# Kernel tuning notes

Hardware: AMD Instinct MI355X
Metric: run time of the kernel (lower is better)

Reference implementation:

```python
import jax, jax.numpy as jnp
import numpy as np

N_NODES = 20000
N_EDGES = 320000
DIM = 256
OUT_DIM = 256
N_LAYERS = 2
AVG_LOG = float(np.log(17.0))  # PNA avg_deg['log'] from deg histogram (all degree 16)
STD_EPS = 1e-5
N_AGG = 5
N_SCALER = 3


def _pna_conv(x, edge_index, Wpre, bpre, Wpost, bpost, Wlin, blin):
    """PyG PNAConv (towers=1, pre_layers=1, post_layers=1, divide_input=False)."""
    N = x.shape[0]
    src, dst = edge_index[0], edge_index[1]  # messages flow src -> dst
    # pre_nn on concat([x_i, x_j]) per edge: [E, 2F] -> [E, F]
    m = jnp.concatenate([x[dst], x[src]], axis=-1) @ Wpre.T + bpre
    deg = jax.ops.segment_sum(jnp.ones((src.shape[0],), x.dtype), dst, num_segments=N)
    degc = jnp.maximum(deg, 1.0)[:, None]
    s = jax.ops.segment_sum(m, dst, num_segments=N)
    mean = s / degc
    mean2 = jax.ops.segment_sum(m * m, dst, num_segments=N) / degc
    std = jnp.sqrt(jax.nn.relu(mean2 - mean * mean) + STD_EPS)
    has = (deg > 0)[:, None]
    mn = jnp.where(has, jax.ops.segment_min(m, dst, num_segments=N), 0.0)
    mx = jnp.where(has, jax.ops.segment_max(m, dst, num_segments=N), 0.0)
    agg = jnp.concatenate([mean, s, std, mn, mx], axis=-1)  # [N, 5F]
    logd = jnp.log(degc + 1.0)
    scaled = jnp.concatenate(
        [agg, agg * (logd / AVG_LOG), agg * (AVG_LOG / logd)], axis=-1)  # [N, 15F]
    h = jnp.concatenate([x, scaled], axis=-1) @ Wpost.T + bpost  # [N, F_out]
    return h @ Wlin.T + blin


def setup_inputs() -> dict:
    key = jax.random.key(0)
    ks = jax.random.split(key, 20)
    F = DIM
    L = N_LAYERS
    post_in = (N_AGG * N_SCALER + 1) * F  # 16F = 4096
    sc = 0.05
    inp = {
        "x": jax.random.normal(ks[0], (N_NODES, F), jnp.float32),
        "edge_index_in": jax.random.randint(ks[1], (2, N_EDGES), 0, N_NODES),
        "edge_index_out": jax.random.randint(ks[2], (2, N_EDGES), 0, N_NODES),
    }
    def p(k, shape):
        return sc * jax.random.normal(k, shape, jnp.float32)
    # stacked per-layer params; supply (_s) and demand (_d) channels
    for tag, base in (("s", 3), ("d", 9)):
        inp[f"Wpre_{tag}"] = p(ks[base + 0], (L, F, 2 * F))
        inp[f"bpre_{tag}"] = p(ks[base + 1], (L, F))
        inp[f"Wpost_{tag}"] = p(ks[base + 2], (L, OUT_DIM, post_in))
        inp[f"bpost_{tag}"] = p(ks[base + 3], (L, OUT_DIM))
        inp[f"Wlin_{tag}"] = p(ks[base + 4], (L, OUT_DIM, OUT_DIM))
        inp[f"blin_{tag}"] = p(ks[base + 5], (L, OUT_DIM))
    inp["Wcomb"] = p(ks[15], (L, OUT_DIM, F + 2 * OUT_DIM))
    inp["bcomb"] = p(ks[16], (L, OUT_DIM))
    inp["Wout"] = p(ks[17], (1, OUT_DIM))
    inp["bout"] = p(ks[18], (1,))
    return inp


def reference(x, edge_index_in, edge_index_out,
              Wpre_s, bpre_s, Wpost_s, bpost_s, Wlin_s, blin_s,
              Wpre_d, bpre_d, Wpost_d, bpost_d, Wlin_d, blin_d,
              Wcomb, bcomb, Wout, bout):
    for l in range(N_LAYERS):
        h_in = jax.nn.relu(_pna_conv(x, edge_index_in,
                                     Wpre_s[l], bpre_s[l], Wpost_s[l], bpost_s[l],
                                     Wlin_s[l], blin_s[l]))
        h_out = jax.nn.relu(_pna_conv(x, edge_index_out,
                                      Wpre_d[l], bpre_d[l], Wpost_d[l], bpost_d[l],
                                      Wlin_d[l], blin_d[l]))
        x = jax.nn.relu(jnp.concatenate([x, h_in, h_out], axis=-1) @ Wcomb[l].T + bcomb[l])
    return jnp.squeeze(x @ Wout.T + bout)  # [N]
```

## Files before the change

### kernel.cpp

```cpp
#include <hip/hip_runtime.h>
#include <math.h>

#define NN 20000
#define NE 320000
#define FD 256
#define AVG_LOG_F 2.83321334f

typedef unsigned short u16;
typedef _Float16 h8_t __attribute__((ext_vector_type(8)));
typedef float f4_t __attribute__((ext_vector_type(4)));

__device__ __forceinline__ u16 f2h(float f) {
  _Float16 h = (_Float16)f;
  return __builtin_bit_cast(u16, h);
}
__device__ __forceinline__ float h2f(u16 u) {
  _Float16 h = __builtin_bit_cast(_Float16, u);
  return (float)h;
}
__device__ __forceinline__ void gld16(const void* g, void* l) {
  __builtin_amdgcn_global_load_lds(
      (const __attribute__((address_space(1))) void*)g,
      (__attribute__((address_space(3))) void*)l, 16, 0, 0);
}

__global__ __launch_bounds__(256) void k_count(const int* __restrict__ dst,
                                               int* __restrict__ deg, int E) {
  int e = blockIdx.x * 256 + threadIdx.x;
  if (e < E) atomicAdd(&deg[dst[e]], 1);
}

__global__ __launch_bounds__(1024) void k_scan(const int* __restrict__ deg,
                                               int* __restrict__ rp, int N) {
  __shared__ int lds[1024];
  int t = threadIdx.x;
  int CH = (N + 1023) >> 10;
  int base = t * CH;
  int s = 0;
  for (int i = 0; i < CH; ++i) { int idx = base + i; if (idx < N) s += deg[idx]; }
  lds[t] = s;
  __syncthreads();
  for (int off = 1; off < 1024; off <<= 1) {
    int v = (t >= off) ? lds[t - off] : 0;
    __syncthreads();
    lds[t] += v;
    __syncthreads();
  }
  int run = (t == 0) ? 0 : lds[t - 1];
  for (int i = 0; i < CH; ++i) {
    int idx = base + i;
    if (idx < N) { rp[idx] = run; run += deg[idx]; }
  }
  if (t == 1023) rp[N] = run;
}

__global__ __launch_bounds__(256) void k_scatter(const int* __restrict__ src,
                                                 const int* __restrict__ dst,
                                                 const int* __restrict__ rp,
                                                 int* __restrict__ cur,
                                                 int* __restrict__ col, int E) {
  int e = blockIdx.x * 256 + threadIdx.x;
  if (e < E) {
    int d = dst[e];
    int p = atomicAdd(&cur[d], 1);
    col[rp[d] + p] = src[e];
  }
}

__global__ __launch_bounds__(256) void k_cvt(const float* __restrict__ in,
                                             u16* __restrict__ out, int n4) {
  int i = blockIdx.x * 256 + threadIdx.x;
  if (i < n4) {
    float4 v = *(const float4*)(in + (size_t)i * 4);
    ushort4 o;
    o.x = f2h(v.x); o.y = f2h(v.y); o.z = f2h(v.z); o.w = f2h(v.w);
    *(ushort4*)(out + (size_t)i * 4) = o;
  }
}

__global__ __launch_bounds__(256) void k_cvtx(const float* __restrict__ x,
                                              u16* __restrict__ xc) {
  int i = blockIdx.x * 256 + threadIdx.x;
  int row = i >> 6, c = (i & 63) * 4;
  float4 v = *(const float4*)(x + (size_t)row * 256 + c);
  ushort4 o;
  o.x = f2h(v.x); o.y = f2h(v.y); o.z = f2h(v.z); o.w = f2h(v.w);
  *(ushort4*)(xc + (size_t)row * 768 + c) = o;
}

__global__ __launch_bounds__(256) void k_tc(const float* __restrict__ in,
                                            u16* __restrict__ out) {
  __shared__ float tile[32][33];
  int bx = blockIdx.x;
  int by = blockIdx.y;
  int r = threadIdx.x >> 5, c = threadIdx.x & 31;
#pragma unroll
  for (int it = 0; it < 4; ++it)
    tile[r + it * 8][c] = in[(size_t)(by * 32 + r + it * 8) * 4096 + bx * 32 + c];
  __syncthreads();
#pragma unroll
  for (int it = 0; it < 4; ++it)
    out[(size_t)(bx * 32 + r + it * 8) * 256 + by * 32 + c] = f2h(tile[c][r + it * 8]);
}

__global__ __launch_bounds__(512) void k_mgemm(
    const u16* __restrict__ A, int lda,
    const u16* __restrict__ B, const u16* __restrict__ B2, int ldb, int nsplit,
    const float* __restrict__ bias, const float* __restrict__ bias2,
    float* __restrict__ oF, int ldoF, int ncutF,
    u16* __restrict__ oH, int ldoH,
    int M, int K, int relu) {
  __shared__ u16 As[64 * 64];
  __shared__ u16 Bs[256 * 64];
  const int t = threadIdx.x;
  const int m0 = blockIdx.y * 64;
  const int n0 = blockIdx.x * 256;
  const int l = t & 63;
  const int w = t >> 6;
  const int wm = w >> 2, wn = w & 3;
  const int lo = l & 15, hi = l >> 4;

  f4_t acc[2][4];
#pragma unroll
  for (int i = 0; i < 2; ++i)
#pragma unroll
    for (int j = 0; j < 4; ++j) acc[i][j] = (f4_t)0.f;

  int ra = t >> 3, pa = t & 7;
  int la = pa ^ (ra & 7);
  int rra = m0 + ra;
  if (rra > M - 1) rra = M - 1;
  const u16* gA = A + (size_t)rra * lda + la * 8;
  u16* lA = &As[t * 8];

  const u16* gB[4];
  u16* lB[4];
#pragma unroll
  for (int i = 0; i < 4; ++i) {
    int q = i * 512 + t;
    int r = q >> 3, p = q & 7;
    int lc = p ^ (r & 7);
    int n = n0 + r;
    const u16* bp = (n < nsplit) ? (B + (size_t)n * ldb)
                                 : (B2 + (size_t)(n - nsplit) * ldb);
    gB[i] = bp + lc * 8;
    lB[i] = &Bs[q * 8];
  }

  for (int k0 = 0; k0 < K; k0 += 64) {
    gld16(gA + k0, lA);
#pragma unroll
    for (int i = 0; i < 4; ++i) gld16(gB[i] + k0, lB[i]);
    __syncthreads();
#pragma unroll
    for (int ks = 0; ks < 2; ++ks) {
      h8_t af[2], bf[4];
#pragma unroll
      for (int mi = 0; mi < 2; ++mi) {
        int row = wm * 32 + mi * 16 + lo;
        int c = (ks * 4 + hi) ^ (row & 7);
        af[mi] = *(const h8_t*)&As[row * 64 + c * 8];
      }
#pragma unroll
      for (int ni = 0; ni < 4; ++ni) {
        int row = wn * 64 + ni * 16 + lo;
        int c = (ks * 4 + hi) ^ (row & 7);
        bf[ni] = *(const h8_t*)&Bs[row * 64 + c * 8];
      }
#pragma unroll
      for (int mi = 0; mi < 2; ++mi)
#pragma unroll
        for (int ni = 0; ni < 4; ++ni)
          acc[mi][ni] = __builtin_amdgcn_mfma_f32_16x16x32_f16(
              af[mi], bf[ni], acc[mi][ni], 0, 0, 0);
    }
    __syncthreads();
  }

  float bv[4];
#pragma unroll
  for (int ni = 0; ni < 4; ++ni) {
    int n = n0 + wn * 64 + ni * 16 + lo;
    bv[ni] = (n < nsplit) ? (bias ? bias[n] : 0.f)
                          : (bias2 ? bias2[n - nsplit] : 0.f);
  }
#pragma unroll
  for (int mi = 0; mi < 2; ++mi) {
#pragma unroll
    for (int r = 0; r < 4; ++r) {
      int m = m0 + wm * 32 + mi * 16 + hi * 4 + r;
      if (m < M) {
#pragma unroll
        for (int ni = 0; ni < 4; ++ni) {
          int n = n0 + wn * 64 + ni * 16 + lo;
          float v = acc[mi][ni][r] + bv[ni];
          if (relu && v < 0.f) v = 0.f;
          if (n < ncutF) {
            oF[(size_t)m * ldoF + n] = v;
          } else {
            oH[(size_t)m * ldoH + (n - ncutF)] = f2h(v);
          }
        }
      }
    }
  }
}

__global__ __launch_bounds__(512) void k_pgemm(
    const u16* __restrict__ xc, const u16* __restrict__ agg5,
    const float* __restrict__ scal3, const u16* __restrict__ Wf,
    const float* __restrict__ bf, u16* __restrict__ oH, int M) {
  __shared__ u16 As[64 * 64];
  __shared__ u16 Bs[256 * 64];
  const int t = threadIdx.x;
  const int m0 = blockIdx.x * 64;
  const int l = t & 63;
  const int w = t >> 6;
  const int wm = w >> 2, wn = w & 3;
  const int lo = l & 15, hi = l >> 4;

  f4_t acc[2][4];
#pragma unroll
  for (int i = 0; i < 2; ++i)
#pragma unroll
    for (int j = 0; j < 4; ++j) acc[i][j] = (f4_t)0.f;

  const int ra = t >> 3, pa = t & 7;
  int m = m0 + ra;
  if (m > M - 1) m = M - 1;
  u16* ldA = &As[ra * 64 + (pa ^ (ra & 7)) * 8];
  const u16* xrow = xc + (size_t)m * 768;
  const u16* arow = agg5 + (size_t)m * 1280;
  const float* srow = scal3 + (size_t)m * 4;

  const u16* gB[4];
  u16* lB[4];
#pragma unroll
  for (int i = 0; i < 4; ++i) {
    int q = i * 512 + t;
    int r = q >> 3, p = q & 7;
    int lc = p ^ (r & 7);
    gB[i] = Wf + (size_t)r * 4096 + lc * 8;
    lB[i] = &Bs[q * 8];
  }

  for (int k0 = 0; k0 < 4096; k0 += 64) {
#pragma unroll
    for (int i = 0; i < 4; ++i) gld16(gB[i] + k0, lB[i]);
    int k = k0 + pa * 8;
    h8_t v;
    if (k < 256) {
      v = *(const h8_t*)(xrow + k);
    } else {
      int q = k - 256;
      int g = q / 1280;
      int r2 = q - g * 1280;
      v = *(const h8_t*)(arow + r2);
      v = v * (_Float16)srow[g];
    }
    *(h8_t*)ldA = v;
    __syncthreads();
#pragma unroll
    for (int ks = 0; ks < 2; ++ks) {
      h8_t af[2], bfr[4];
#pragma unroll
      for (int mi = 0; mi < 2; ++mi) {
        int row = wm * 32 + mi * 16 + lo;
        int c = (ks * 4 + hi) ^ (row & 7);
        af[mi] = *(const h8_t*)&As[row * 64 + c * 8];
      }
#pragma unroll
      for (int ni = 0; ni < 4; ++ni) {
        int row = wn * 64 + ni * 16 + lo;
        int c = (ks * 4 + hi) ^ (row & 7);
        bfr[ni] = *(const h8_t*)&Bs[row * 64 + c * 8];
      }
#pragma unroll
      for (int mi = 0; mi < 2; ++mi)
#pragma unroll
        for (int ni = 0; ni < 4; ++ni)
          acc[mi][ni] = __builtin_amdgcn_mfma_f32_16x16x32_f16(
              af[mi], bfr[ni], acc[mi][ni], 0, 0, 0);
    }
    __syncthreads();
  }

  float bv[4];
#pragma unroll
  for (int ni = 0; ni < 4; ++ni) bv[ni] = bf[wn * 64 + ni * 16 + lo];
#pragma unroll
  for (int mi = 0; mi < 2; ++mi) {
#pragma unroll
    for (int r = 0; r < 4; ++r) {
      int mr = m0 + wm * 32 + mi * 16 + hi * 4 + r;
      if (mr < M) {
#pragma unroll
        for (int ni = 0; ni < 4; ++ni) {
          int n = wn * 64 + ni * 16 + lo;
          float vv = acc[mi][ni][r] + bv[ni];
          if (vv < 0.f) vv = 0.f;
          oH[(size_t)mr * 768 + n] = f2h(vv);
        }
      }
    }
  }
}

__global__ __launch_bounds__(256) void k_aggregate(
    const float* __restrict__ A, const u16* __restrict__ Bh,
    const int* __restrict__ rp, const int* __restrict__ col,
    u16* __restrict__ agg5, float* __restrict__ scal3) {
  int w = threadIdx.x >> 6, l = threadIdx.x & 63;
  int n = blockIdx.x * 4 + w;
  int beg = rp[n], end = rp[n + 1];
  int deg = end - beg;
  float sb[4] = {0.f, 0.f, 0.f, 0.f}, qb[4] = {0.f, 0.f, 0.f, 0.f};
  float mnb[4], mxb[4];
#pragma unroll
  for (int j = 0; j < 4; ++j) { mnb[j] = 3.402823466e38f; mxb[j] = -3.402823466e38f; }
  for (int i = beg; i < end; ++i) {
    int s = col[i];
    ushort4 bv = *(const ushort4*)(Bh + (size_t)s * FD + l * 4);
    float b[4] = {h2f(bv.x), h2f(bv.y), h2f(bv.z), h2f(bv.w)};
#pragma unroll
    for (int j = 0; j < 4; ++j) {
      sb[j] += b[j];
      qb[j] = fmaf(b[j], b[j], qb[j]);
      mnb[j] = fminf(mnb[j], b[j]);
      mxb[j] = fmaxf(mxb[j], b[j]);
    }
  }
  float4 c4 = *(const float4*)(A + (size_t)n * FD + l * 4);
  float cc[4] = {c4.x, c4.y, c4.z, c4.w};
  float degf = (float)deg;
  float degc = degf > 1.f ? degf : 1.f;
  float inv = 1.f / degc;
  float outv[5][4];
#pragma unroll
  for (int j = 0; j < 4; ++j) {
    float c = cc[j];
    float s_m = fmaf(degf, c, sb[j]);
    float mean = s_m * inv;
    float mean2 = fmaf(degf * c, c, fmaf(2.f * c, sb[j], qb[j])) * inv;
    float var = mean2 - mean * mean;
    if (var < 0.f) var = 0.f;
    float sd = sqrtf(var + 1e-5f);
    outv[0][j] = mean;
    outv[1][j] = s_m;
    outv[2][j] = sd;
    outv[3][j] = deg > 0 ? c + mnb[j] : 0.f;
    outv[4][j] = deg > 0 ? c + mxb[j] : 0.f;
  }
  u16* base = agg5 + (size_t)n * 1280 + l * 4;
#pragma unroll
  for (int a = 0; a < 5; ++a) {
    ushort4 o;
    o.x = f2h(outv[a][0]);
    o.y = f2h(outv[a][1]);
    o.z = f2h(outv[a][2]);
    o.w = f2h(outv[a][3]);
    *(ushort4*)(base + a * 256) = o;
  }
  if (l == 0) {
    float logd = logf(degc + 1.f);
    scal3[(size_t)n * 4 + 0] = 1.f;
    scal3[(size_t)n * 4 + 1] = logd / AVG_LOG_F;
    scal3[(size_t)n * 4 + 2] = AVG_LOG_F / logd;
    scal3[(size_t)n * 4 + 3] = 0.f;
  }
}

__global__ __launch_bounds__(256) void k_bfuse(const float* __restrict__ Wlin,
                                               const float* __restrict__ bpost,
                                               const float* __restrict__ blin,
                                               float* __restrict__ bf) {
  __shared__ float bp[256];
  int t = threadIdx.x;
  bp[t] = bpost[t];
  __syncthreads();
  float s = blin[t];
  for (int k = 0; k < 256; ++k) s = fmaf(Wlin[t * 256 + k], bp[k], s);
  bf[t] = s;
}

__global__ __launch_bounds__(256) void k_wout(const u16* __restrict__ x,
                                              const float* __restrict__ w,
                                              const float* __restrict__ b,
                                              float* __restrict__ out, int N) {
  int wid = threadIdx.x >> 6, lane = threadIdx.x & 63;
  int n = blockIdx.x * 4 + wid;
  if (n >= N) return;
  ushort4 xv = *(const ushort4*)(x + (size_t)n * FD + lane * 4);
  const float4 wv = *(const float4*)(w + lane * 4);
  float s = h2f(xv.x) * wv.x + h2f(xv.y) * wv.y + h2f(xv.z) * wv.z + h2f(xv.w) * wv.w;
#pragma unroll
  for (int off = 32; off > 0; off >>= 1) s += __shfl_down(s, off);
  if (lane == 0) out[n] = s + b[0];
}

extern "C" void kernel_launch(void* const* d_in, const int* in_sizes, int n_in,
                              void* d_out, int out_size, void* d_ws, size_t ws_size,
                              hipStream_t stream) {
  const float* x0      = (const float*)d_in[0];
  const int*   ei_in   = (const int*)d_in[1];
  const int*   ei_out  = (const int*)d_in[2];
  const float* Wpre_s  = (const float*)d_in[3];
  const float* bpre_s  = (const float*)d_in[4];
  const float* Wpost_s = (const float*)d_in[5];
  const float* bpost_s = (const float*)d_in[6];
  const float* Wlin_s  = (const float*)d_in[7];
  const float* blin_s  = (const float*)d_in[8];
  const float* Wpre_d  = (const float*)d_in[9];
  const float* bpre_d  = (const float*)d_in[10];
  const float* Wpost_d = (const float*)d_in[11];
  const float* bpost_d = (const float*)d_in[12];
  const float* Wlin_d  = (const float*)d_in[13];
  const float* blin_d  = (const float*)d_in[14];
  const float* Wcomb   = (const float*)d_in[15];
  const float* bcomb   = (const float*)d_in[16];
  const float* Wout    = (const float*)d_in[17];
  const float* bout    = (const float*)d_in[18];
  float* out = (float*)d_out;

  char* p = (char*)d_ws;
  auto alloc = [&](size_t b) {
    char* r = p;
    p += (b + 255) & ~(size_t)255;
    return r;
  };
  int* deg      = (int*)alloc((size_t)NN * 4);
  int* cur      = (int*)alloc((size_t)NN * 4);
  int* rp_in    = (int*)alloc((size_t)(NN + 1) * 4);
  int* col_in   = (int*)alloc((size_t)NE * 4);
  int* rp_out   = (int*)alloc((size_t)(NN + 1) * 4);
  int* col_out  = (int*)alloc((size_t)NE * 4);
  float* Abuf   = (float*)alloc((size_t)NN * FD * 4);
  u16* Bbuf     = (u16*)alloc((size_t)NN * FD * 2);
  u16* agg5     = (u16*)alloc((size_t)NN * 1280 * 2);
  float* scal3  = (float*)alloc((size_t)NN * 4 * 4);
  u16* xcat1    = (u16*)alloc((size_t)NN * 768 * 2);
  u16* xcat2    = (u16*)alloc((size_t)NN * 768 * 2);
  u16* xfin     = (u16*)alloc((size_t)NN * FD * 2);
  u16* Wpre_sb  = (u16*)alloc((size_t)2 * 256 * 512 * 2);
  u16* Wpre_db  = (u16*)alloc((size_t)2 * 256 * 512 * 2);
  u16* Wlin_sb  = (u16*)alloc((size_t)2 * 256 * 256 * 2);
  u16* Wlin_db  = (u16*)alloc((size_t)2 * 256 * 256 * 2);
  u16* Wcomb_b  = (u16*)alloc((size_t)2 * 256 * 768 * 2);
  u16* WpostT   = (u16*)alloc((size_t)4096 * 256 * 2);
  u16* Wf       = (u16*)alloc((size_t)256 * 4096 * 2);
  float* bfv    = (float*)alloc((size_t)256 * 4);

  const int EB = (NE + 255) / 256;
  const int BIG = 1 << 30;

  k_cvt<<<256, 256, 0, stream>>>(Wpre_s, Wpre_sb, 65536);
  k_cvt<<<256, 256, 0, stream>>>(Wpre_d, Wpre_db, 65536);
  k_cvt<<<128, 256, 0, stream>>>(Wlin_s, Wlin_sb, 32768);
  k_cvt<<<128, 256, 0, stream>>>(Wlin_d, Wlin_db, 32768);
  k_cvt<<<384, 256, 0, stream>>>(Wcomb, Wcomb_b, 98304);
  k_cvtx<<<5000, 256, 0, stream>>>(x0, xcat1);

  hipMemsetAsync(deg, 0, (size_t)NN * 4, stream);
  k_count<<<EB, 256, 0, stream>>>(ei_in + NE, deg, NE);
  k_scan<<<1, 1024, 0, stream>>>(deg, rp_in, NN);
  hipMemsetAsync(cur, 0, (size_t)NN * 4, stream);
  k_scatter<<<EB, 256, 0, stream>>>(ei_in, ei_in + NE, rp_in, cur, col_in, NE);
  hipMemsetAsync(deg, 0, (size_t)NN * 4, stream);
  k_count<<<EB, 256, 0, stream>>>(ei_out + NE, deg, NE);
  k_scan<<<1, 1024, 0, stream>>>(deg, rp_out, NN);
  hipMemsetAsync(cur, 0, (size_t)NN * 4, stream);
  k_scatter<<<EB, 256, 0, stream>>>(ei_out, ei_out + NE, rp_out, cur, col_out, NE);

  u16* xcats[2] = {xcat1, xcat2};
  for (int lyr = 0; lyr < 2; ++lyr) {
    u16* xc = xcats[lyr];
    for (int c = 0; c < 2; ++c) {
      const float* bpre  = (c == 0) ? bpre_s : bpre_d;
      const float* Wpost = (c == 0) ? Wpost_s : Wpost_d;
      const float* bpost = (c == 0) ? bpost_s : bpost_d;
      const float* Wlin  = (c == 0) ? Wlin_s : Wlin_d;
      const float* blin  = (c == 0) ? blin_s : blin_d;
      u16* Wpre_b = (c == 0) ? Wpre_sb : Wpre_db;
      u16* Wlin_b = (c == 0) ? Wlin_sb : Wlin_db;
      const int* rp  = (c == 0) ? rp_in : rp_out;
      const int* col = (c == 0) ? col_in : col_out;

      k_mgemm<<<dim3(2, 313), 512, 0, stream>>>(
          xc, 768,
          Wpre_b + (size_t)lyr * 131072, Wpre_b + (size_t)lyr * 131072 + 256, 512, 256,
          bpre + (size_t)lyr * 256, nullptr,
          Abuf, 256, 256,
          Bbuf, 256,
          NN, 256, 0);
      k_aggregate<<<5000, 256, 0, stream>>>(Abuf, Bbuf, rp, col, agg5, scal3);
      k_tc<<<dim3(128, 8), 256, 0, stream>>>(Wpost + (size_t)lyr * 256 * 4096, WpostT);
      k_mgemm<<<dim3(16, 4), 512, 0, stream>>>(
          Wlin_b + (size_t)lyr * 65536, 256,
          WpostT, WpostT, 256, BIG,
          nullptr, nullptr,
          nullptr, 0, 0,
          Wf, 4096,
          256, 256, 0);
      k_bfuse<<<1, 256, 0, stream>>>(Wlin + (size_t)lyr * 65536,
                                     bpost + (size_t)lyr * 256,
                                     blin + (size_t)lyr * 256, bfv);
      k_pgemm<<<dim3(313), 512, 0, stream>>>(
          xc, agg5, scal3, Wf, bfv, xc + 256 + c * 256, NN);
    }
    if (lyr == 0) {
      k_mgemm<<<dim3(1, 313), 512, 0, stream>>>(
          xc, 768,
          Wcomb_b, Wcomb_b, 768, BIG,
          bcomb, nullptr,
          nullptr, 0, 0,
          xcat2, 768,
          NN, 768, 1);
    } else {
      k_mgemm<<<dim3(1, 313), 512, 0, stream>>>(
          xc, 768,
          Wcomb_b + 196608, Wcomb_b + 196608, 768, BIG,
          bcomb + 256, nullptr,
          nullptr, 0, 0,
          xfin, 256,
          NN, 768, 1);
    }
  }
  k_wout<<<5000, 256, 0, stream>>>(xfin, Wout, bout, out, NN);
}
```

Measured before the change: 937.6 us.

## Batch setup kernels, double-buffer GEMMs, fuse channels, fp16 pre-GEMM outputs

Merges the weight conversions, degree counting, CSR scatter, Wpost transposes, weight folding and bias folding into single batched launches covering both channels and both layers. Adds LDS double buffering to the GEMM and post-GEMM kernels so global loads overlap with MFMA work. Runs both channels' post-GEMMs in one launch. The pre-GEMM now writes both halves in fp16, and the aggregation reads 8 halves per lane with two edges in flight per wave. The trade-offs are lower precision in the center term, double the LDS per block (possibly lower occupancy), and buffer aliasing (WpostT4 in agg52, xfin in xcat1) that relies on stream ordering.

After: 852.4 us. 9.1% less time.

```diff
diff --git a/kernel.cpp b/kernel.cpp
--- a/kernel.cpp
+++ b/kernel.cpp
@@ -3,7 +3,6 @@
 
 #define NN 20000
 #define NE 320000
-#define FD 256
 #define AVG_LOG_F 2.83321334f
 
 typedef unsigned short u16;
@@ -13,10 +12,6 @@
 __device__ __forceinline__ u16 f2h(float f) {
   _Float16 h = (_Float16)f;
   return __builtin_bit_cast(u16, h);
-}
-__device__ __forceinline__ float h2f(u16 u) {
-  _Float16 h = __builtin_bit_cast(_Float16, u);
-  return (float)h;
 }
 __device__ __forceinline__ void gld16(const void* g, void* l) {
   __builtin_amdgcn_global_load_lds(
@@ -24,10 +19,13 @@
       (__attribute__((address_space(3))) void*)l, 16, 0, 0);
 }
 
-__global__ __launch_bounds__(256) void k_count(const int* __restrict__ dst,
-                                               int* __restrict__ deg, int E) {
+__global__ __launch_bounds__(256) void k_count2(const int* __restrict__ ein,
+                                                const int* __restrict__ eout,
+                                                int* __restrict__ deg2, int E) {
   int e = blockIdx.x * 256 + threadIdx.x;
-  if (e < E) atomicAdd(&deg[dst[e]], 1);
+  int ch = blockIdx.y;
+  const int* dst = (ch ? eout : ein) + E;
+  if (e < E) atomicAdd(&deg2[ch * NN + dst[e]], 1);
 }
 
 __global__ __launch_bounds__(1024) void k_scan(const int* __restrict__ deg,
@@ -54,28 +52,44 @@
   if (t == 1023) rp[N] = run;
 }
 
-__global__ __launch_bounds__(256) void k_scatter(const int* __restrict__ src,
-                                                 const int* __restrict__ dst,
-                                                 const int* __restrict__ rp,
-                                                 int* __restrict__ cur,
-                                                 int* __restrict__ col, int E) {
+__global__ __launch_bounds__(256) void k_scatter2(const int* __restrict__ ein,
+                                                  const int* __restrict__ eout,
+                                                  const int* __restrict__ rp2,
+                                                  int* __restrict__ cur2,
+                                                  int* __restrict__ col2, int E) {
   int e = blockIdx.x * 256 + threadIdx.x;
+  int ch = blockIdx.y;
+  const int* src = (ch ? eout : ein);
+  const int* dst = src + E;
   if (e < E) {
     int d = dst[e];
-    int p = atomicAdd(&cur[d], 1);
-    col[rp[d] + p] = src[e];
-  }
-}
-
-__global__ __launch_bounds__(256) void k_cvt(const float* __restrict__ in,
-                                             u16* __restrict__ out, int n4) {
+    int p = atomicAdd(&cur2[ch * NN + d], 1);
+    col2[rp2[ch * NN + d] + p] = src[e];
+  }
+}
+
+__global__ __launch_bounds__(256) void k_cvtw(
+    const float* __restrict__ Wpre_s, const float* __restrict__ Wpre_d,
+    const float* __restrict__ Wlin_s, const float* __restrict__ Wlin_d,
+    const float* __restrict__ Wcomb,
+    u16* __restrict__ preS, u16* __restrict__ preD,
+    u16* __restrict__ lincat, u16* __restrict__ combB) {
   int i = blockIdx.x * 256 + threadIdx.x;
-  if (i < n4) {
-    float4 v = *(const float4*)(in + (size_t)i * 4);
-    ushort4 o;
-    o.x = f2h(v.x); o.y = f2h(v.y); o.z = f2h(v.z); o.w = f2h(v.w);
-    *(ushort4*)(out + (size_t)i * 4) = o;
-  }
+  const float* src;
+  u16* dst;
+  int so, dofs;
+  if (i < 65536)       { src = Wpre_s; dst = preS;  so = i;          dofs = so; }
+  else if (i < 131072) { src = Wpre_d; dst = preD;  so = i - 65536;  dofs = so; }
+  else if (i < 163840) { int j = i - 131072; int lyr = j >> 14;
+                         src = Wlin_s; dst = lincat; so = j; dofs = j + lyr * 16384; }
+  else if (i < 196608) { int j = i - 163840; int lyr = j >> 14;
+                         src = Wlin_d; dst = lincat; so = j; dofs = j + (lyr + 1) * 16384; }
+  else if (i < 294912) { src = Wcomb; dst = combB; so = i - 196608; dofs = so; }
+  else return;
+  float4 v = *(const float4*)(src + (size_t)so * 4);
+  ushort4 o;
+  o.x = f2h(v.x); o.y = f2h(v.y); o.z = f2h(v.z); o.w = f2h(v.w);
+  *(ushort4*)(dst + (size_t)dofs * 4) = o;
 }
 
 __global__ __launch_bounds__(256) void k_cvtx(const float* __restrict__ x,
@@ -88,11 +102,14 @@
   *(ushort4*)(xc + (size_t)row * 768 + c) = o;
 }
 
-__global__ __launch_bounds__(256) void k_tc(const float* __restrict__ in,
-                                            u16* __restrict__ out) {
+__global__ __launch_bounds__(256) void k_tc4(const float* __restrict__ Ws,
+                                             const float* __restrict__ Wd,
+                                             u16* __restrict__ outT) {
   __shared__ float tile[32][33];
-  int bx = blockIdx.x;
-  int by = blockIdx.y;
+  int z = blockIdx.z;
+  const float* in = ((z & 1) ? Wd : Ws) + (size_t)(z >> 1) * 256 * 4096;
+  u16* out = outT + (size_t)z * (4096 * 256);
+  int bx = blockIdx.x, by = blockIdx.y;
   int r = threadIdx.x >> 5, c = threadIdx.x & 31;
 #pragma unroll
   for (int it = 0; it < 4; ++it)
@@ -106,17 +123,20 @@
 __global__ __launch_bounds__(512) void k_mgemm(
     const u16* __restrict__ A, int lda,
     const u16* __restrict__ B, const u16* __restrict__ B2, int ldb, int nsplit,
-    const float* __restrict__ bias, const float* __restrict__ bias2,
-    float* __restrict__ oF, int ldoF, int ncutF,
+    const float* __restrict__ bias,
     u16* __restrict__ oH, int ldoH,
-    int M, int K, int relu) {
-  __shared__ u16 As[64 * 64];
-  __shared__ u16 Bs[256 * 64];
+    int M, int K, int relu, int zA, int zB, int zO) {
+  __shared__ u16 As[2][64 * 64];
+  __shared__ u16 Bs[2][256 * 64];
   const int t = threadIdx.x;
+  const int z = blockIdx.z;
+  A += (size_t)z * zA;
+  B += (size_t)z * zB;
+  B2 += (size_t)z * zB;
+  oH += (size_t)z * zO;
   const int m0 = blockIdx.y * 64;
   const int n0 = blockIdx.x * 256;
-  const int l = t & 63;
-  const int w = t >> 6;
+  const int l = t & 63, w = t >> 6;
   const int wm = w >> 2, wn = w & 3;
   const int lo = l & 15, hi = l >> 4;
 
@@ -126,53 +146,60 @@
 #pragma unroll
     for (int j = 0; j < 4; ++j) acc[i][j] = (f4_t)0.f;
 
-  int ra = t >> 3, pa = t & 7;
-  int la = pa ^ (ra & 7);
+  const int ra = t >> 3, pa = t & 7;
+  const int la = pa ^ (ra & 7);
   int rra = m0 + ra;
   if (rra > M - 1) rra = M - 1;
   const u16* gA = A + (size_t)rra * lda + la * 8;
-  u16* lA = &As[t * 8];
 
   const u16* gB[4];
-  u16* lB[4];
+  int lBo[4];
 #pragma unroll
   for (int i = 0; i < 4; ++i) {
     int q = i * 512 + t;
-    int r = q >> 3, p = q & 7;
-    int lc = p ^ (r & 7);
+    int r = q >> 3, p2 = q & 7;
+    int lc = p2 ^ (r & 7);
     int n = n0 + r;
-    const u16* bp = (n < nsplit) ? (B + (size_t)n * ldb)
-                                 : (B2 + (size_t)(n - nsplit) * ldb);
+    const u16* bp = (n < nsplit) ? (B + (size_t)n * ldb) : (B2 + (size_t)(n - nsplit) * ldb);
     gB[i] = bp + lc * 8;
-    lB[i] = &Bs[q * 8];
-  }
-
-  for (int k0 = 0; k0 < K; k0 += 64) {
-    gld16(gA + k0, lA);
-#pragma unroll
-    for (int i = 0; i < 4; ++i) gld16(gB[i] + k0, lB[i]);
-    __syncthreads();
+    lBo[i] = q * 8;
+  }
+
+  gld16(gA, &As[0][t * 8]);
+#pragma unroll
+  for (int i = 0; i < 4; ++i) gld16(gB[i], &Bs[0][lBo[i]]);
+  __syncthreads();
+
+  const int nt = K >> 6;
+  for (int tt = 0; tt < nt; ++tt) {
+    const int cur = tt & 1;
+    if (tt + 1 < nt) {
+      const int ko = (tt + 1) << 6;
+      gld16(gA + ko, &As[cur ^ 1][t * 8]);
+#pragma unroll
+      for (int i = 0; i < 4; ++i) gld16(gB[i] + ko, &Bs[cur ^ 1][lBo[i]]);
+    }
 #pragma unroll
     for (int ks = 0; ks < 2; ++ks) {
-      h8_t af[2], bf[4];
+      h8_t af[2], bfr[4];
 #pragma unroll
       for (int mi = 0; mi < 2; ++mi) {
         int row = wm * 32 + mi * 16 + lo;
         int c = (ks * 4 + hi) ^ (row & 7);
-        af[mi] = *(const h8_t*)&As[row * 64 + c * 8];
+        af[mi] = *(const h8_t*)&As[cur][row * 64 + c * 8];
       }
 #pragma unroll
       for (int ni = 0; ni < 4; ++ni) {
         int row = wn * 64 + ni * 16 + lo;
         int c = (ks * 4 + hi) ^ (row & 7);
-        bf[ni] = *(const h8_t*)&Bs[row * 64 + c * 8];
+        bfr[ni] = *(const h8_t*)&Bs[cur][row * 64 + c * 8];
       }
 #pragma unroll
       for (int mi = 0; mi < 2; ++mi)
 #pragma unroll
         for (int ni = 0; ni < 4; ++ni)
           acc[mi][ni] = __builtin_amdgcn_mfma_f32_16x16x32_f16(
-              af[mi], bf[ni], acc[mi][ni], 0, 0, 0);
+              af[mi], bfr[ni], acc[mi][ni], 0, 0, 0);
     }
     __syncthreads();
   }
@@ -181,8 +208,7 @@
 #pragma unroll
   for (int ni = 0; ni < 4; ++ni) {
     int n = n0 + wn * 64 + ni * 16 + lo;
-    bv[ni] = (n < nsplit) ? (bias ? bias[n] : 0.f)
-                          : (bias2 ? bias2[n - nsplit] : 0.f);
+    bv[ni] = (n < nsplit) ? (bias ? bias[n] : 0.f) : 0.f;
   }
 #pragma unroll
   for (int mi = 0; mi < 2; ++mi) {
@@ -195,11 +221,7 @@
           int n = n0 + wn * 64 + ni * 16 + lo;
           float v = acc[mi][ni][r] + bv[ni];
           if (relu && v < 0.f) v = 0.f;
-          if (n < ncutF) {
-            oF[(size_t)m * ldoF + n] = v;
-          } else {
-            oH[(size_t)m * ldoH + (n - ncutF)] = f2h(v);
-          }
+          oH[(size_t)m * ldoH + n] = f2h(v);
         }
       }
     }
@@ -207,15 +229,20 @@
 }
 
 __global__ __launch_bounds__(512) void k_pgemm(
-    const u16* __restrict__ xc, const u16* __restrict__ agg5,
-    const float* __restrict__ scal3, const u16* __restrict__ Wf,
-    const float* __restrict__ bf, u16* __restrict__ oH, int M) {
-  __shared__ u16 As[64 * 64];
-  __shared__ u16 Bs[256 * 64];
+    const u16* __restrict__ xc, const u16* __restrict__ agg5c,
+    const float* __restrict__ scal3c, const u16* __restrict__ Wfl,
+    const float* __restrict__ bfl, u16* __restrict__ oHb, int M) {
+  __shared__ u16 As[2][64 * 64];
+  __shared__ u16 Bs[2][256 * 64];
   const int t = threadIdx.x;
+  const int ch = blockIdx.y;
+  const u16* agg5 = agg5c + (size_t)ch * NN * 1280;
+  const float* scal3 = scal3c + (size_t)ch * NN * 4;
+  const u16* Wf = Wfl + (size_t)ch * (256 * 4096);
+  const float* bf = bfl + ch * 256;
+  u16* oH = oHb + 256 + ch * 256;
   const int m0 = blockIdx.x * 64;
-  const int l = t & 63;
-  const int w = t >> 6;
+  const int l = t & 63, w = t >> 6;
   const int wm = w >> 2, wn = w & 3;
   const int lo = l & 15, hi = l >> 4;
 
@@ -228,38 +255,50 @@
   const int ra = t >> 3, pa = t & 7;
   int m = m0 + ra;
   if (m > M - 1) m = M - 1;
-  u16* ldA = &As[ra * 64 + (pa ^ (ra & 7)) * 8];
   const u16* xrow = xc + (size_t)m * 768;
   const u16* arow = agg5 + (size_t)m * 1280;
-  const float* srow = scal3 + (size_t)m * 4;
+  const float s1 = scal3[(size_t)m * 4 + 1];
+  const float s2 = scal3[(size_t)m * 4 + 2];
+  const int aslot = ra * 64 + (pa ^ (ra & 7)) * 8;
 
   const u16* gB[4];
-  u16* lB[4];
+  int lBo[4];
 #pragma unroll
   for (int i = 0; i < 4; ++i) {
     int q = i * 512 + t;
-    int r = q >> 3, p = q & 7;
-    int lc = p ^ (r & 7);
+    int r = q >> 3, p2 = q & 7;
+    int lc = p2 ^ (r & 7);
     gB[i] = Wf + (size_t)r * 4096 + lc * 8;
-    lB[i] = &Bs[q * 8];
-  }
-
-  for (int k0 = 0; k0 < 4096; k0 += 64) {
-#pragma unroll
-    for (int i = 0; i < 4; ++i) gld16(gB[i] + k0, lB[i]);
-    int k = k0 + pa * 8;
-    h8_t v;
-    if (k < 256) {
-      v = *(const h8_t*)(xrow + k);
-    } else {
-      int q = k - 256;
-      int g = q / 1280;
-      int r2 = q - g * 1280;
-      v = *(const h8_t*)(arow + r2);
-      v = v * (_Float16)srow[g];
-    }
-    *(h8_t*)ldA = v;
-    __syncthreads();
+    lBo[i] = q * 8;
+  }
+
+  {
+    h8_t va = *(const h8_t*)(xrow + pa * 8);
+#pragma unroll
+    for (int i = 0; i < 4; ++i) gld16(gB[i], &Bs[0][lBo[i]]);
+    *(h8_t*)&As[0][aslot] = va;
+  }
+  __syncthreads();
+
+  for (int tt = 0; tt < 64; ++tt) {
+    const int cur = tt & 1;
+    h8_t va2 = (h8_t)(_Float16)0.f;
+    float fac = 1.f;
+    if (tt < 63) {
+      int k = ((tt + 1) << 6) + pa * 8;
+      const u16* ap;
+      if (k < 256) {
+        ap = xrow + k;
+      } else {
+        int q = k - 256;
+        int r2 = q < 1280 ? q : (q < 2560 ? q - 1280 : q - 2560);
+        fac = q < 1280 ? 1.f : (q < 2560 ? s1 : s2);
+        ap = arow + r2;
+      }
+      va2 = *(const h8_t*)ap;
+#pragma unroll
+      for (int i = 0; i < 4; ++i) gld16(gB[i] + ((tt + 1) << 6), &Bs[cur ^ 1][lBo[i]]);
+    }
 #pragma unroll
     for (int ks = 0; ks < 2; ++ks) {
       h8_t af[2], bfr[4];
@@ -267,13 +306,13 @@
       for (int mi = 0; mi < 2; ++mi) {
         int row = wm * 32 + mi * 16 + lo;
         int c = (ks * 4 + hi) ^ (row & 7);
-        af[mi] = *(const h8_t*)&As[row * 64 + c * 8];
+        af[mi] = *(const h8_t*)&As[cur][row * 64 + c * 8];
       }
 #pragma unroll
       for (int ni = 0; ni < 4; ++ni) {
         int row = wn * 64 + ni * 16 + lo;
         int c = (ks * 4 + hi) ^ (row & 7);
-        bfr[ni] = *(const h8_t*)&Bs[row * 64 + c * 8];
+        bfr[ni] = *(const h8_t*)&Bs[cur][row * 64 + c * 8];
       }
 #pragma unroll
       for (int mi = 0; mi < 2; ++mi)
@@ -282,6 +321,7 @@
           acc[mi][ni] = __builtin_amdgcn_mfma_f32_16x16x32_f16(
               af[mi], bfr[ni], acc[mi][ni], 0, 0, 0);
     }
+    if (tt < 63) *(h8_t*)&As[cur ^ 1][aslot] = va2 * (_Float16)fac;
     __syncthreads();
   }
 
@@ -307,80 +347,92 @@
 }
 
 __global__ __launch_bounds__(256) void k_aggregate(
-    const float* __restrict__ A, const u16* __restrict__ Bh,
-    const int* __restrict__ rp, const int* __restrict__ col,
-    u16* __restrict__ agg5, float* __restrict__ scal3) {
+    const u16* __restrict__ AB, const int* __restrict__ rp,
+    const int* __restrict__ col, u16* __restrict__ agg5,
+    float* __restrict__ scal3) {
   int w = threadIdx.x >> 6, l = threadIdx.x & 63;
   int n = blockIdx.x * 4 + w;
   int beg = rp[n], end = rp[n + 1];
   int deg = end - beg;
-  float sb[4] = {0.f, 0.f, 0.f, 0.f}, qb[4] = {0.f, 0.f, 0.f, 0.f};
-  float mnb[4], mxb[4];
-#pragma unroll
-  for (int j = 0; j < 4; ++j) { mnb[j] = 3.402823466e38f; mxb[j] = -3.402823466e38f; }
-  for (int i = beg; i < end; ++i) {
+  int half = l >> 5, lf = l & 31;
+  float sb[8], qb[8], mnb[8], mxb[8];
+#pragma unroll
+  for (int j = 0; j < 8; ++j) {
+    sb[j] = 0.f; qb[j] = 0.f;
+    mnb[j] = 3.402823466e38f; mxb[j] = -3.402823466e38f;
+  }
+  for (int i = beg + half; i < end; i += 2) {
     int s = col[i];
-    ushort4 bv = *(const ushort4*)(Bh + (size_t)s * FD + l * 4);
-    float b[4] = {h2f(bv.x), h2f(bv.y), h2f(bv.z), h2f(bv.w)};
-#pragma unroll
-    for (int j = 0; j < 4; ++j) {
-      sb[j] += b[j];
-      qb[j] = fmaf(b[j], b[j], qb[j]);
-      mnb[j] = fminf(mnb[j], b[j]);
-      mxb[j] = fmaxf(mxb[j], b[j]);
-    }
-  }
-  float4 c4 = *(const float4*)(A + (size_t)n * FD + l * 4);
-  float cc[4] = {c4.x, c4.y, c4.z, c4.w};
+    h8_t bv = *(const h8_t*)(AB + (size_t)s * 512 + 256 + lf * 8);
+#pragma unroll
+    for (int j = 0; j < 8; ++j) {
+      float b = (float)bv[j];
+      sb[j] += b;
+      qb[j] = fmaf(b, b, qb[j]);
+      mnb[j] = fminf(mnb[j], b);
+      mxb[j] = fmaxf(mxb[j], b);
+    }
+  }
+#pragma unroll
+  for (int j = 0; j < 8; ++j) {
+    sb[j] += __shfl_xor(sb[j], 32, 64);
+    qb[j] += __shfl_xor(qb[j], 32, 64);
+    mnb[j] = fminf(mnb[j], __shfl_xor(mnb[j], 32, 64));
+    mxb[j] = fmaxf(mxb[j], __shfl_xor(mxb[j], 32, 64));
+  }
+  h8_t cv = *(const h8_t*)(AB + (size_t)n * 512 + lf * 8);
   float degf = (float)deg;
   float degc = degf > 1.f ? degf : 1.f;
   float inv = 1.f / degc;
-  float outv[5][4];
-#pragma unroll
-  for (int j = 0; j < 4; ++j) {
-    float c = cc[j];
+  float ov[5][8];
+#pragma unroll
+  for (int j = 0; j < 8; ++j) {
+    float c = (float)cv[j];
     float s_m = fmaf(degf, c, sb[j]);
     float mean = s_m * inv;
     float mean2 = fmaf(degf * c, c, fmaf(2.f * c, sb[j], qb[j])) * inv;
     float var = mean2 - mean * mean;
     if (var < 0.f) var = 0.f;
     float sd = sqrtf(var + 1e-5f);
-    outv[0][j] = mean;
-    outv[1][j] = s_m;
-    outv[2][j] = sd;
-    outv[3][j] = deg > 0 ? c + mnb[j] : 0.f;
-    outv[4][j] = deg > 0 ? c + mxb[j] : 0.f;
-  }
-  u16* base = agg5 + (size_t)n * 1280 + l * 4;
-#pragma unroll
-  for (int a = 0; a < 5; ++a) {
-    ushort4 o;
-    o.x = f2h(outv[a][0]);
-    o.y = f2h(outv[a][1]);
-    o.z = f2h(outv[a][2]);
-    o.w = f2h(outv[a][3]);
-    *(ushort4*)(base + a * 256) = o;
-  }
-  if (l == 0) {
-    float logd = logf(degc + 1.f);
-    scal3[(size_t)n * 4 + 0] = 1.f;
-    scal3[(size_t)n * 4 + 1] = logd / AVG_LOG_F;
-    scal3[(size_t)n * 4 + 2] = AVG_LOG_F / logd;
-    scal3[(size_t)n * 4 + 3] = 0.f;
-  }
-}
-
-__global__ __launch_bounds__(256) void k_bfuse(const float* __restrict__ Wlin,
-                                               const float* __restrict__ bpost,
-                                               const float* __restrict__ blin,
-                                               float* __restrict__ bf) {
+    ov[0][j] = mean;
+    ov[1][j] = s_m;
+    ov[2][j] = sd;
+    ov[3][j] = deg > 0 ? c + mnb[j] : 0.f;
+    ov[4][j] = deg > 0 ? c + mxb[j] : 0.f;
+  }
+  if (half == 0) {
+    u16* base = agg5 + (size_t)n * 1280 + lf * 8;
+#pragma unroll
+    for (int a = 0; a < 5; ++a) {
+      h8_t o;
+#pragma unroll
+      for (int j = 0; j < 8; ++j) o[j] = (_Float16)ov[a][j];
+      *(h8_t*)(base + a * 256) = o;
+    }
+    if (lf == 0) {
+      float logd = logf(degc + 1.f);
+      float4 sc = make_float4(1.f, logd / AVG_LOG_F, AVG_LOG_F / logd, 0.f);
+      *(float4*)(scal3 + (size_t)n * 4) = sc;
+    }
+  }
+}
+
+__global__ __launch_bounds__(256) void k_bfuse4(
+    const float* __restrict__ Wlin_s, const float* __restrict__ Wlin_d,
+    const float* __restrict__ bpost_s, const float* __restrict__ bpost_d,
+    const float* __restrict__ blin_s, const float* __restrict__ blin_d,
+    float* __restrict__ bfv4) {
   __shared__ float bp[256];
+  int z = blockIdx.x, lyr = z >> 1, ch = z & 1;
+  const float* Wlin = (ch ? Wlin_d : Wlin_s) + (size_t)lyr * 65536;
+  const float* bpost = (ch ? bpost_d : bpost_s) + lyr * 256;
+  const float* blin = (ch ? blin_d : blin_s) + lyr * 256;
   int t = threadIdx.x;
   bp[t] = bpost[t];
   __syncthreads();
   float s = blin[t];
   for (int k = 0; k < 256; ++k) s = fmaf(Wlin[t * 256 + k], bp[k], s);
-  bf[t] = s;
+  bfv4[z * 256 + t] = s;
 }
 
 __global__ __launch_bounds__(256) void k_wout(const u16* __restrict__ x,
@@ -390,9 +442,12 @@
   int wid = threadIdx.x >> 6, lane = threadIdx.x & 63;
   int n = blockIdx.x * 4 + wid;
   if (n >= N) return;
-  ushort4 xv = *(const ushort4*)(x + (size_t)n * FD + lane * 4);
+  ushort4 xv = *(const ushort4*)(x + (size_t)n * 256 + lane * 4);
   const float4 wv = *(const float4*)(w + lane * 4);
-  float s = h2f(xv.x) * wv.x + h2f(xv.y) * wv.y + h2f(xv.z) * wv.z + h2f(xv.w) * wv.w;
+  float s = (float)__builtin_bit_cast(_Float16, xv.x) * wv.x +
+            (float)__builtin_bit_cast(_Float16, xv.y) * wv.y +
+            (float)__builtin_bit_cast(_Float16, xv.z) * wv.z +
+            (float)__builtin_bit_cast(_Float16, xv.w) * wv.w;
 #pragma unroll
   for (int off = 32; off > 0; off >>= 1) s += __shfl_down(s, off);
   if (lane == 0) out[n] = s + b[0];
@@ -428,101 +483,63 @@
     p += (b + 255) & ~(size_t)255;
     return r;
   };
-  int* deg      = (int*)alloc((size_t)NN * 4);
-  int* cur      = (int*)alloc((size_t)NN * 4);
-  int* rp_in    = (int*)alloc((size_t)(NN + 1) * 4);
-  int* col_in   = (int*)alloc((size_t)NE * 4);
-  int* rp_out   = (int*)alloc((size_t)(NN + 1) * 4);
-  int* col_out  = (int*)alloc((size_t)NE * 4);
-  float* Abuf   = (float*)alloc((size_t)NN * FD * 4);
-  u16* Bbuf     = (u16*)alloc((size_t)NN * FD * 2);
-  u16* agg5     = (u16*)alloc((size_t)NN * 1280 * 2);
-  float* scal3  = (float*)alloc((size_t)NN * 4 * 4);
+  int* deg2     = (int*)alloc((size_t)2 * NN * 4);
+  int* cur2     = (int*)alloc((size_t)2 * NN * 4);
+  int* rp2      = (int*)alloc((size_t)(2 * NN + 1) * 4);
+  int* col2     = (int*)alloc((size_t)2 * NE * 4);
+  u16* AB       = (u16*)alloc((size_t)NN * 512 * 2);
+  u16* agg52    = (u16*)alloc((size_t)2 * NN * 1280 * 2);
+  float* scal32 = (float*)alloc((size_t)2 * NN * 4 * 4);
   u16* xcat1    = (u16*)alloc((size_t)NN * 768 * 2);
   u16* xcat2    = (u16*)alloc((size_t)NN * 768 * 2);
-  u16* xfin     = (u16*)alloc((size_t)NN * FD * 2);
-  u16* Wpre_sb  = (u16*)alloc((size_t)2 * 256 * 512 * 2);
-  u16* Wpre_db  = (u16*)alloc((size_t)2 * 256 * 512 * 2);
-  u16* Wlin_sb  = (u16*)alloc((size_t)2 * 256 * 256 * 2);
-  u16* Wlin_db  = (u16*)alloc((size_t)2 * 256 * 256 * 2);
-  u16* Wcomb_b  = (u16*)alloc((size_t)2 * 256 * 768 * 2);
-  u16* WpostT   = (u16*)alloc((size_t)4096 * 256 * 2);
-  u16* Wf       = (u16*)alloc((size_t)256 * 4096 * 2);
-  float* bfv    = (float*)alloc((size_t)256 * 4);
-
-  const int EB = (NE + 255) / 256;
+  u16* preS     = (u16*)alloc((size_t)2 * 256 * 512 * 2);
+  u16* preD     = (u16*)alloc((size_t)2 * 256 * 512 * 2);
+  u16* lincat   = (u16*)alloc((size_t)4 * 256 * 256 * 2);
+  u16* combB    = (u16*)alloc((size_t)2 * 256 * 768 * 2);
+  u16* Wf4      = (u16*)alloc((size_t)4 * 256 * 4096 * 2);
+  float* bfv4   = (float*)alloc((size_t)4 * 256 * 4);
+  u16* WpostT4  = (u16*)agg52;
+  u16* xfin     = xcat1;
+
   const int BIG = 1 << 30;
 
-  k_cvt<<<256, 256, 0, stream>>>(Wpre_s, Wpre_sb, 65536);
-  k_cvt<<<256, 256, 0, stream>>>(Wpre_d, Wpre_db, 65536);
-  k_cvt<<<128, 256, 0, stream>>>(Wlin_s, Wlin_sb, 32768);
-  k_cvt<<<128, 256, 0, stream>>>(Wlin_d, Wlin_db, 32768);
-  k_cvt<<<384, 256, 0, stream>>>(Wcomb, Wcomb_b, 98304);
+  k_cvtw<<<1152, 256, 0, stream>>>(Wpre_s, Wpre_d, Wlin_s, Wlin_d, Wcomb,
+                                   preS, preD, lincat, combB);
   k_cvtx<<<5000, 256, 0, stream>>>(x0, xcat1);
-
-  hipMemsetAsync(deg, 0, (size_t)NN * 4, stream);
-  k_count<<<EB, 256, 0, stream>>>(ei_in + NE, deg, NE);
-  k_scan<<<1, 1024, 0, stream>>>(deg, rp_in, NN);
-  hipMemsetAsync(cur, 0, (size_t)NN * 4, stream);
-  k_scatter<<<EB, 256, 0, stream>>>(ei_in, ei_in + NE, rp_in, cur, col_in, NE);
-  hipMemsetAsync(deg, 0, (size_t)NN * 4, stream);
-  k_count<<<EB, 256, 0, stream>>>(ei_out + NE, deg, NE);
-  k_scan<<<1, 1024, 0, stream>>>(deg, rp_out, NN);
-  hipMemsetAsync(cur, 0, (size_t)NN * 4, stream);
-  k_scatter<<<EB, 256, 0, stream>>>(ei_out, ei_out + NE, rp_out, cur, col_out, NE);
-
-  u16* xcats[2] = {xcat1, xcat2};
+  hipMemsetAsync(deg2, 0, (size_t)4 * NN * 4, stream);
+  k_count2<<<dim3(1250, 2), 256, 0, stream>>>(ei_in, ei_out, deg2, NE);
+  k_scan<<<1, 1024, 0, stream>>>(deg2, rp2, 2 * NN);
+  k_scatter2<<<dim3(1250, 2), 256, 0, stream>>>(ei_in, ei_out, rp2, cur2, col2, NE);
+  k_tc4<<<dim3(128, 8, 4), 256, 0, stream>>>(Wpost_s, Wpost_d, WpostT4);
+  k_mgemm<<<dim3(16, 4, 4), 512, 0, stream>>>(
+      lincat, 256, WpostT4, WpostT4, 256, BIG, nullptr,
+      Wf4, 4096, 256, 256, 0, 65536, 1048576, 1048576);
+  k_bfuse4<<<4, 256, 0, stream>>>(Wlin_s, Wlin_d, bpost_s, bpost_d, blin_s, blin_d, bfv4);
+
+  u16* xcs[2] = {xcat1, xcat2};
   for (int lyr = 0; lyr < 2; ++lyr) {
-    u16* xc = xcats[lyr];
-    for (int c = 0; c < 2; ++c) {
-      const float* bpre  = (c == 0) ? bpre_s : bpre_d;
-      const float* Wpost = (c == 0) ? Wpost_s : Wpost_d;
-      const float* bpost = (c == 0) ? bpost_s : bpost_d;
-      const float* Wlin  = (c == 0) ? Wlin_s : Wlin_d;
-      const float* blin  = (c == 0) ? blin_s : blin_d;
-      u16* Wpre_b = (c == 0) ? Wpre_sb : Wpre_db;
-      u16* Wlin_b = (c == 0) ? Wlin_sb : Wlin_db;
-      const int* rp  = (c == 0) ? rp_in : rp_out;
-      const int* col = (c == 0) ? col_in : col_out;
-
-      k_mgemm<<<dim3(2, 313), 512, 0, stream>>>(
-          xc, 768,
-          Wpre_b + (size_t)lyr * 131072, Wpre_b + (size_t)lyr * 131072 + 256, 512, 256,
-          bpre + (size_t)lyr * 256, nullptr,
-          Abuf, 256, 256,
-          Bbuf, 256,
-          NN, 256, 0);
-      k_aggregate<<<5000, 256, 0, stream>>>(Abuf, Bbuf, rp, col, agg5, scal3);
-      k_tc<<<dim3(128, 8), 256, 0, stream>>>(Wpost + (size_t)lyr * 256 * 4096, WpostT);
-      k_mgemm<<<dim3(16, 4), 512, 0, stream>>>(
-          Wlin_b + (size_t)lyr * 65536, 256,
-          WpostT, WpostT, 256, BIG,
-          nullptr, nullptr,
-          nullptr, 0, 0,
-          Wf, 4096,
-          256, 256, 0);
-      k_bfuse<<<1, 256, 0, stream>>>(Wlin + (size_t)lyr * 65536,
-                                     bpost + (size_t)lyr * 256,
-                                     blin + (size_t)lyr * 256, bfv);
-      k_pgemm<<<dim3(313), 512, 0, stream>>>(
-          xc, agg5, scal3, Wf, bfv, xc + 256 + c * 256, NN);
-    }
+    u16* xc = xcs[lyr];
+    for (int ch = 0; ch < 2; ++ch) {
+      u16* preW = ch ? preD : preS;
+      const float* bpre = ch ? bpre_d : bpre_s;
+      k_mgemm<<<dim3(2, 313, 1), 512, 0, stream>>>(
+          xc, 768, preW + (size_t)lyr * 131072, preW + (size_t)lyr * 131072 + 256,
+          512, 256, bpre + (size_t)lyr * 256,
+          AB, 512, NN, 256, 0, 0, 0, 0);
+      k_aggregate<<<5000, 256, 0, stream>>>(
+          AB, rp2 + ch * NN, col2,
+          agg52 + (size_t)ch * NN * 1280, scal32 + (size_t)ch * NN * 4);
+    }
+    k_pgemm<<<dim3(313, 2), 512, 0, stream>>>(
+        xc, agg52, scal32, Wf4 + (size_t)lyr * 2 * 1048576, bfv4 + lyr * 512, xc, NN);
     if (lyr == 0) {
-      k_mgemm<<<dim3(1, 313), 512, 0, stream>>>(
-          xc, 768,
-          Wcomb_b, Wcomb_b, 768, BIG,
-          bcomb, nullptr,
-          nullptr, 0, 0,
-          xcat2, 768,
-          NN, 768, 1);
+      k_mgemm<<<dim3(1, 313, 1), 512, 0, stream>>>(
+          xc, 768, combB, combB, 768, BIG, bcomb,
+          xcat2, 768, NN, 768, 1, 0, 0, 0);
     } else {
-      k_mgemm<<<dim3(1, 313), 512, 0, stream>>>(
-          xc, 768,
-          Wcomb_b + 196608, Wcomb_b + 196608, 768, BIG,
-          bcomb + 256, nullptr,
-          nullptr, 0, 0,
-          xfin, 256,
-          NN, 768, 1);
+      k_mgemm<<<dim3(1, 313, 1), 512, 0, stream>>>(
+          xc, 768, combB + 196608, combB + 196608, 768, BIG, bcomb + 256,
+          xfin, 256, NN, 768, 1, 0, 0, 0);
     }
   }
   k_wout<<<5000, 256, 0, stream>>>(xfin, Wout, bout, out, NN);
```
